# Performance work log

Hardware: AMD Instinct MI355X
Metric: run time of the kernel (lower is better)

Reference implementation:

```python
import jax, jax.numpy as jnp
import numpy as np

N_NODES = 20000
E_RAND = 300000
IN_F, OUT_F, HEADS = 1280, 128, 4
HID = OUT_F * HEADS  # 512


def gat_conv(x, src, dst, W, attn_l, attn_r, bias, n_nodes):
    """DGL GATConv: fc (no bias) -> per-edge LeakyReLU(el_src+er_dst) ->
    segment softmax over incoming edges -> weighted scatter-sum -> +bias.
    Returns (N, HEADS, OUT_F)."""
    h = (x @ W).reshape(n_nodes, HEADS, OUT_F)            # (N,H,F)
    el = jnp.einsum('nhf,hf->nh', h, attn_l)              # (N,H)
    er = jnp.einsum('nhf,hf->nh', h, attn_r)              # (N,H)
    e = jax.nn.leaky_relu(el[src] + er[dst], 0.2)         # (E,H)
    emax = jax.ops.segment_max(e, dst, num_segments=n_nodes)
    ee = jnp.exp(e - emax[dst])                           # (E,H)
    denom = jax.ops.segment_sum(ee, dst, num_segments=n_nodes)
    alpha = ee / denom[dst]                               # (E,H)
    msg = h[src] * alpha[:, :, None]                      # (E,H,F)
    out = jax.ops.segment_sum(msg, dst, num_segments=n_nodes)
    return out + bias.reshape(HEADS, OUT_F)


def setup_inputs() -> dict:
    key = jax.random.key(0)
    ks = jax.random.split(key, 12)
    src_r = jax.random.randint(ks[0], (E_RAND,), 0, N_NODES)
    dst_r = jax.random.randint(ks[1], (E_RAND,), 0, N_NODES)
    self_loop = jnp.arange(N_NODES)
    src = jnp.concatenate([src_r, self_loop])  # self loops: contact[i][i]=1
    dst = jnp.concatenate([dst_r, self_loop])
    feature = jax.random.normal(ks[2], (N_NODES, IN_F), dtype=jnp.float32)
    s1 = 1.0 / np.sqrt(IN_F)
    s2 = 1.0 / np.sqrt(HID)
    return {
        'feature': feature,
        'W1': jax.random.normal(ks[3], (IN_F, HID), dtype=jnp.float32) * s1,
        'al1': jax.random.normal(ks[4], (HEADS, OUT_F), dtype=jnp.float32) * s2,
        'ar1': jax.random.normal(ks[5], (HEADS, OUT_F), dtype=jnp.float32) * s2,
        'b1': jnp.zeros((HID,), dtype=jnp.float32),
        'W2': jax.random.normal(ks[6], (HID, HID), dtype=jnp.float32) * s2,
        'al2': jax.random.normal(ks[7], (HEADS, OUT_F), dtype=jnp.float32) * s2,
        'ar2': jax.random.normal(ks[8], (HEADS, OUT_F), dtype=jnp.float32) * s2,
        'b2': jnp.zeros((HID,), dtype=jnp.float32),
        'Wfc': jax.random.normal(ks[9], (HID, 64), dtype=jnp.float32) * s2,
        'bfc': jnp.zeros((64,), dtype=jnp.float32),
        'src': src,
        'dst': dst,
    }


def reference(feature, W1, al1, ar1, b1, W2, al2, ar2, b2, Wfc, bfc, src, dst):
    n = feature.shape[0]
    out = gat_conv(feature, src, dst, W1, al1, ar1, b1, n)   # (N,4,128)
    out = jax.nn.elu(out).reshape(n, HID)                    # (N,512)
    out = gat_conv(out, src, dst, W2, al2, ar2, b2, n)       # (N,4,128)
    out = jax.nn.elu(out).reshape(n, HID)                    # (N,512)
    out = out @ Wfc + bfc                                    # (N,64)
    out = jax.nn.elu(out[None, :, :])                        # (1,N,64)
    return out
```

## Files before the change

kernel.cpp:

```cpp
#include <hip/hip_runtime.h>
#include <hip/hip_bf16.h>
#include <math.h>

#define HID 512
#define HEADS 4
#define OUTF 128

typedef __attribute__((ext_vector_type(8))) _Float16 f16x8_t;
typedef __attribute__((ext_vector_type(4))) _Float16 f16x4_t;
typedef __attribute__((ext_vector_type(4))) float f32x4_t;

__device__ __forceinline__ void gl_lds16(const void* g, void* l) {
    __builtin_amdgcn_global_load_lds(
        (const __attribute__((address_space(1))) void*)g,
        (__attribute__((address_space(3))) void*)l, 16, 0, 0);
}

__device__ __forceinline__ void stage_plane32(const _Float16* g, int strideE,
    int rbase, int rmax, char* plane, int tid)
{
#pragma unroll
    for (int j = 0; j < 2; ++j) {
        int gci = j * 256 + tid;
        int r = gci >> 2, c = gci & 3;
        int rg = rbase + r; if (rg > rmax) rg = rmax;
        const char* s = (const char*)(g + (size_t)rg * strideE) + ((c ^ ((r >> 1) & 3)) << 4);
        char* d = plane + (j * 256 + (tid & ~63)) * 16;
        gl_lds16(s, d);
    }
}

__device__ __forceinline__ void a32_load(const float* g, int strideE,
    int rbase, int rmax, int tid, int kbase, float4* v)
{
#pragma unroll
    for (int j = 0; j < 2; ++j) {
        int gci = j * 256 + tid;
        int r = gci >> 2, c = gci & 3;
        int rg = rbase + r; if (rg > rmax) rg = rmax;
        const float* s = g + (size_t)rg * strideE + kbase + ((c ^ ((r >> 1) & 3)) << 3);
        v[j * 2]     = *(const float4*)s;
        v[j * 2 + 1] = *(const float4*)(s + 4);
    }
}
__device__ __forceinline__ void a32_write(char* plane, int tid, const float4* v)
{
#pragma unroll
    for (int j = 0; j < 2; ++j) {
        const float4 a = v[j * 2], b = v[j * 2 + 1];
        f16x8_t o;
        o[0] = (_Float16)a.x; o[1] = (_Float16)a.y;
        o[2] = (_Float16)a.z; o[3] = (_Float16)a.w;
        o[4] = (_Float16)b.x; o[5] = (_Float16)b.y;
        o[6] = (_Float16)b.z; o[7] = (_Float16)b.w;
        *(f16x8_t*)(plane + (j * 256 + tid) * 16) = o;
    }
}

__global__ __launch_bounds__(256) void prep_w(const float* __restrict__ W,
    _Float16* __restrict__ Wt, int K, int NC)
{
    __shared__ float tile[32][33];
    const int k0 = blockIdx.x * 32, n0 = blockIdx.y * 32;
    const int t = threadIdx.x;
    {
        int r = t >> 3, c4 = (t & 7) * 4;
        float4 v = *(const float4*)&W[(size_t)(k0 + r) * NC + n0 + c4];
        tile[r][c4] = v.x; tile[r][c4 + 1] = v.y;
        tile[r][c4 + 2] = v.z; tile[r][c4 + 3] = v.w;
    }
    __syncthreads();
    int n = t >> 3, kc = (t & 7) * 4;
#pragma unroll
    for (int i = 0; i < 4; ++i)
        Wt[(size_t)(n0 + n) * K + k0 + kc + i] = (_Float16)tile[kc + i][n];
}

template<int EPI, int OUT16, int ELER, int A32>
__global__ __launch_bounds__(256, 3) void gemm_f16(
    const void* __restrict__ Ap, const _Float16* __restrict__ Bt,
    const float* __restrict__ bias,
    const float* __restrict__ attl, const float* __restrict__ attr,
    float* __restrict__ elp, float* __restrict__ erp,
    void* __restrict__ Cout, int M, int K, int NCOL, int ldC,
    int ncolT, int nwg)
{
    __shared__ char lds[32768];
    const _Float16* Af  = (const _Float16*)Ap;
    const float*    Af32 = (const float*)Ap;
    const int tid = threadIdx.x;
    const int wave = tid >> 6, lane = tid & 63;
    const int wm = wave >> 1, wn = wave & 1;
    const int b = blockIdx.x;
    const int q = nwg >> 3, rr = nwg & 7;
    const int xcd = b & 7, ib = b >> 3;
    const int logical = (xcd < rr ? xcd * (q + 1) : rr * (q + 1) + (xcd - rr) * q) + ib;
    const int bm = (logical / ncolT) * 128, bcol = logical % ncolT;
    const int bn = bcol * 128;
    const int l15 = lane & 15, l4 = lane >> 4;
    const int swz = (l15 >> 1) & 3;

    f32x4_t acc[4][4];
#pragma unroll
    for (int i = 0; i < 4; ++i)
#pragma unroll
        for (int j = 0; j < 4; ++j) acc[i][j] = (f32x4_t){0.f, 0.f, 0.f, 0.f};

    const int nt = K >> 5;
    float4 pre[4];
    if (A32) {
        a32_load(Af32, K, bm, M - 1, tid, 0, pre);
        a32_write(lds, tid, pre);
    } else {
        stage_plane32(Af, K, bm, M - 1, lds, tid);
    }
    stage_plane32(Bt, K, bn, NCOL - 1, lds + 8192, tid);
    __syncthreads();

    for (int t = 0; t < nt; ++t) {
        char* AH = lds + (t & 1) * 16384;
        char* BH = AH + 8192;
        char* AHn = lds + ((t + 1) & 1) * 16384;
        if (t + 1 < nt) {
            if (A32) a32_load(Af32, K, bm, M - 1, tid, (t + 1) * 32, pre);
            else     stage_plane32(Af + (t + 1) * 32, K, bm, M - 1, AHn, tid);
            stage_plane32(Bt + (t + 1) * 32, K, bn, NCOL - 1, AHn + 8192, tid);
        }
        f16x8_t fa[4], fb[4];
#pragma unroll
        for (int mf = 0; mf < 4; ++mf) {
            int row = wm * 64 + mf * 16 + l15;
            fa[mf] = *(const f16x8_t*)(AH + row * 64 + ((l4 ^ swz) << 4));
        }
#pragma unroll
        for (int nf = 0; nf < 4; ++nf) {
            int rn = wn * 64 + nf * 16 + l15;
            fb[nf] = *(const f16x8_t*)(BH + rn * 64 + ((l4 ^ swz) << 4));
        }
#pragma unroll
        for (int mf = 0; mf < 4; ++mf)
#pragma unroll
            for (int nf = 0; nf < 4; ++nf)
                acc[mf][nf] = __builtin_amdgcn_mfma_f32_16x16x32_f16(fa[mf], fb[nf], acc[mf][nf], 0, 0, 0);
        if (A32 && t + 1 < nt) a32_write(AHn, tid, pre);
        __syncthreads();
    }
#pragma unroll
    for (int mf = 0; mf < 4; ++mf) {
        int rbase = bm + wm * 64 + mf * 16 + l4 * 4;
#pragma unroll
        for (int nf = 0; nf < 4; ++nf) {
            int col = bn + wn * 64 + nf * 16 + l15;
            if (col >= NCOL) continue;
#pragma unroll
            for (int r = 0; r < 4; ++r) {
                int row = rbase + r;
                if (row < M) {
                    float v = acc[mf][nf][r];
                    if (EPI) {
                        v += bias[col];
                        v = v > 0.f ? v : (expf(v) - 1.f);
                    }
                    if (OUT16) ((_Float16*)Cout)[(size_t)row * ldC + col] = (_Float16)v;
                    else       ((float*)Cout)[(size_t)row * ldC + col] = v;
                }
            }
        }
    }
    if (ELER) {
        const int head = bcol;
        float alv[4], arv[4];
#pragma unroll
        for (int nf = 0; nf < 4; ++nf) {
            int cl = wn * 64 + nf * 16 + l15;
            alv[nf] = attl[head * OUTF + cl];
            arv[nf] = attr[head * OUTF + cl];
        }
        float pel[4][4], perr[4][4];
#pragma unroll
        for (int mf = 0; mf < 4; ++mf)
#pragma unroll
            for (int r = 0; r < 4; ++r) {
                float se = 0.f, sr = 0.f;
#pragma unroll
                for (int nf = 0; nf < 4; ++nf) {
                    se = fmaf(acc[mf][nf][r], alv[nf], se);
                    sr = fmaf(acc[mf][nf][r], arv[nf], sr);
                }
                pel[mf][r] = se; perr[mf][r] = sr;
            }
#pragma unroll
        for (int off = 1; off < 16; off <<= 1)
#pragma unroll
            for (int mf = 0; mf < 4; ++mf)
#pragma unroll
                for (int r = 0; r < 4; ++r) {
                    pel[mf][r]  += __shfl_xor(pel[mf][r],  off);
                    perr[mf][r] += __shfl_xor(perr[mf][r], off);
                }
        __syncthreads();
        float* red = (float*)lds;
        if (l15 == 0) {
#pragma unroll
            for (int mf = 0; mf < 4; ++mf)
#pragma unroll
                for (int r = 0; r < 4; ++r) {
                    int rl = wm * 64 + mf * 16 + l4 * 4 + r;
                    red[rl * 2 + wn]       = pel[mf][r];
                    red[256 + rl * 2 + wn] = perr[mf][r];
                }
        }
        __syncthreads();
        if (tid < 128) {
            int row = bm + tid;
            if (row < M) {
                float es = red[tid * 2] + red[tid * 2 + 1];
                float rs = red[256 + tid * 2] + red[256 + tid * 2 + 1];
                elp[row * HEADS + head] = es;
                erp[row * HEADS + head] = rs;
            }
        }
    }
}

__global__ void hist_kernel(const int* __restrict__ dst, int* __restrict__ deg, int E)
{
    int e = blockIdx.x * 256 + threadIdx.x;
    if (e < E) atomicAdd(&deg[dst[e]], 1);
}

__global__ __launch_bounds__(256) void scan1_kernel(const int* __restrict__ deg,
    int* __restrict__ offs, int* __restrict__ bsum, int N)
{
    __shared__ int buf[256];
    int tid = threadIdx.x;
    int i = blockIdx.x * 256 + tid;
    int v = (i < N) ? deg[i] : 0;
    buf[tid] = v;
    __syncthreads();
#pragma unroll
    for (int off = 1; off < 256; off <<= 1) {
        int t = (tid >= off) ? buf[tid - off] : 0;
        __syncthreads();
        buf[tid] += t;
        __syncthreads();
    }
    if (i < N) offs[i] = buf[tid] - v;
    if (tid == 255) bsum[blockIdx.x] = buf[255];
}

__global__ void scan2_kernel(int* __restrict__ bsum, int nb)
{
    if (threadIdx.x == 0) {
        int acc = 0;
        for (int b = 0; b < nb; ++b) { int t = bsum[b]; bsum[b] = acc; acc += t; }
        bsum[nb] = acc;
    }
}

__global__ void scan3_kernel(int* __restrict__ offs, const int* __restrict__ bsum,
                             int N, int nb)
{
    int i = blockIdx.x * 256 + threadIdx.x;
    if (i < N) offs[i] += bsum[blockIdx.x];
    if (i == 0) offs[N] = bsum[nb];
}

__global__ void fill_kernel(const int* __restrict__ srcv, const int* __restrict__ dstv,
    const int* __restrict__ offs, int* __restrict__ cursor,
    int* __restrict__ psrc, int E)
{
    int e = blockIdx.x * 256 + threadIdx.x;
    if (e < E) {
        int d = dstv[e];
        int p = atomicAdd(&cursor[d], 1);
        psrc[offs[d] + p] = srcv[e];
    }
}

__global__ __launch_bounds__(256) void aggregate_kernel(const _Float16* __restrict__ h,
    const int* __restrict__ offs, const int* __restrict__ psrc,
    const float* __restrict__ el, const float* __restrict__ er,
    const float* __restrict__ bias, _Float16* __restrict__ xo, int N)
{
    const int n = blockIdx.x * 4 + (threadIdx.x >> 6);
    if (n >= N) return;
    const int lane = threadIdx.x & 63;
    const int c = lane * 8;
    const int head = lane >> 4;
    const int hp = lane >> 5;
    const int e31 = lane & 31;
    const int sbase = (head >> 1) << 5;
    const int hsel = head & 1;

    const float2 er2 = *(const float2*)&er[n * HEADS + hp * 2];

    float acc[8];
#pragma unroll
    for (int k = 0; k < 8; ++k) acc[k] = 0.f;
    float ws = 0.f;

    const int beg = offs[n], end = offs[n + 1];
    for (int base = beg; base < end; base += 32) {
        const int cnt = min(32, end - base);
        int idx = base + e31;
        if (e31 >= cnt) idx = beg;
        const int s = psrc[idx];
        const float2 lv = *(const float2*)&el[s * HEADS + hp * 2];
        float x0 = lv.x + er2.x; x0 = x0 > 0.f ? x0 : 0.2f * x0;
        float x1 = lv.y + er2.y; x1 = x1 > 0.f ? x1 : 0.2f * x1;
        const float wa = expf(x0);
        const float wb = expf(x1);

        int j = 0;
        for (; j + 4 <= cnt; j += 4) {
            int s0 = __shfl(s, j);     int s1 = __shfl(s, j + 1);
            int s2 = __shfl(s, j + 2); int s3 = __shfl(s, j + 3);
            float a0 = __shfl(wa, sbase + j),     b0 = __shfl(wb, sbase + j);
            float a1 = __shfl(wa, sbase + j + 1), b1 = __shfl(wb, sbase + j + 1);
            float a2 = __shfl(wa, sbase + j + 2), b2 = __shfl(wb, sbase + j + 2);
            float a3 = __shfl(wa, sbase + j + 3), b3 = __shfl(wb, sbase + j + 3);
            float w0 = hsel ? b0 : a0;
            float w1 = hsel ? b1 : a1;
            float w2 = hsel ? b2 : a2;
            float w3 = hsel ? b3 : a3;
            f16x8_t v0 = *(const f16x8_t*)&h[(size_t)s0 * HID + c];
            f16x8_t v1 = *(const f16x8_t*)&h[(size_t)s1 * HID + c];
            f16x8_t v2 = *(const f16x8_t*)&h[(size_t)s2 * HID + c];
            f16x8_t v3 = *(const f16x8_t*)&h[(size_t)s3 * HID + c];
#pragma unroll
            for (int k = 0; k < 8; ++k) {
                acc[k] = fmaf(w0, (float)v0[k], acc[k]);
                acc[k] = fmaf(w1, (float)v1[k], acc[k]);
                acc[k] = fmaf(w2, (float)v2[k], acc[k]);
                acc[k] = fmaf(w3, (float)v3[k], acc[k]);
            }
            ws += w0 + w1 + w2 + w3;
        }
        for (; j < cnt; ++j) {
            int s0 = __shfl(s, j);
            float a0 = __shfl(wa, sbase + j), b0 = __shfl(wb, sbase + j);
            float w0 = hsel ? b0 : a0;
            f16x8_t v0 = *(const f16x8_t*)&h[(size_t)s0 * HID + c];
#pragma unroll
            for (int k = 0; k < 8; ++k) acc[k] = fmaf(w0, (float)v0[k], acc[k]);
            ws += w0;
        }
    }
    float inv = 1.f / ws;
    float4 b0v = *(const float4*)&bias[c];
    float4 b1v = *(const float4*)&bias[c + 4];
    float bb[8] = {b0v.x, b0v.y, b0v.z, b0v.w, b1v.x, b1v.y, b1v.z, b1v.w};
    f16x8_t ov;
#pragma unroll
    for (int k = 0; k < 8; ++k) {
        float r = acc[k] * inv + bb[k];
        r = r > 0.f ? r : (expf(r) - 1.f);
        ov[k] = (_Float16)r;
    }
    *(f16x8_t*)&xo[(size_t)n * HID + c] = ov;
}

extern "C" void kernel_launch(void* const* d_in, const int* in_sizes, int n_in,
                              void* d_out, int out_size, void* d_ws, size_t ws_size,
                              hipStream_t stream)
{
    const float* feature = (const float*)d_in[0];
    const float* W1  = (const float*)d_in[1];
    const float* al1 = (const float*)d_in[2];
    const float* ar1 = (const float*)d_in[3];
    const float* b1  = (const float*)d_in[4];
    const float* W2  = (const float*)d_in[5];
    const float* al2 = (const float*)d_in[6];
    const float* ar2 = (const float*)d_in[7];
    const float* b2  = (const float*)d_in[8];
    const float* Wfc = (const float*)d_in[9];
    const float* bfc = (const float*)d_in[10];
    const int* src = (const int*)d_in[11];
    const int* dst = (const int*)d_in[12];
    const int N = in_sizes[0] / 1280;
    const int E = in_sizes[11];
    const int nb = (N + 255) / 256;
    float* out = (float*)d_out;

    char* ws = (char*)d_ws;
    size_t off = 0;
    auto alloc = [&](size_t bytes) {
        void* p = ws + off;
        off += (bytes + 255) & ~(size_t)255;
        return p;
    };
    int* deg    = (int*)alloc((size_t)N * 4);
    int* cursor = (int*)alloc((size_t)N * 4);
    int* offs   = (int*)alloc((size_t)(N + 1) * 4);
    int* bsum   = (int*)alloc((size_t)(nb + 1) * 4);
    float* el   = (float*)alloc((size_t)N * HEADS * 4);
    float* er   = (float*)alloc((size_t)N * HEADS * 4);
    int* psrc   = (int*)alloc((size_t)E * 4);
    _Float16* hbuf  = (_Float16*)alloc((size_t)N * HID * 2);
    _Float16* xh    = (_Float16*)alloc((size_t)N * HID * 2);
    _Float16* W1t   = (_Float16*)alloc((size_t)HID * 1280 * 2);
    _Float16* W2t   = (_Float16*)alloc((size_t)HID * HID * 2);
    _Float16* Wft   = (_Float16*)alloc((size_t)64 * HID * 2);

    hipMemsetAsync(deg, 0, (size_t)N * 4, stream);
    hipMemsetAsync(cursor, 0, (size_t)N * 4, stream);
    hist_kernel<<<(E + 255) / 256, 256, 0, stream>>>(dst, deg, E);
    scan1_kernel<<<nb, 256, 0, stream>>>(deg, offs, bsum, N);
    scan2_kernel<<<1, 64, 0, stream>>>(bsum, nb);
    scan3_kernel<<<nb, 256, 0, stream>>>(offs, bsum, N, nb);
    fill_kernel<<<(E + 255) / 256, 256, 0, stream>>>(src, dst, offs, cursor, psrc, E);

    prep_w<<<dim3(1280 / 32, HID / 32), 256, 0, stream>>>(W1, W1t, 1280, HID);
    prep_w<<<dim3(HID / 32, HID / 32), 256, 0, stream>>>(W2, W2t, HID, HID);
    prep_w<<<dim3(HID / 32, 64 / 32), 256, 0, stream>>>(Wfc, Wft, HID, 64);

    const int nrowT = (N + 127) / 128;
    const int nwgG = nrowT * (HID / 128);
    const int nwgF = nrowT;
    const int aggB = (N + 3) / 4;

    gemm_f16<0, 1, 1, 1><<<nwgG, 256, 0, stream>>>(feature, W1t, nullptr,
                                                   al1, ar1, el, er,
                                                   hbuf, N, 1280, HID, HID,
                                                   HID / 128, nwgG);
    aggregate_kernel<<<aggB, 256, 0, stream>>>(hbuf, offs, psrc, el, er, b1, xh, N);

    gemm_f16<0, 1, 1, 0><<<nwgG, 256, 0, stream>>>(xh, W2t, nullptr,
                                                   al2, ar2, el, er,
                                                   hbuf, N, HID, HID, HID,
                                                   HID / 128, nwgG);
    aggregate_kernel<<<aggB, 256, 0, stream>>>(hbuf, offs, psrc, el, er, b2, xh, N);

    gemm_f16<1, 0, 0, 0><<<nwgF, 256, 0, stream>>>(xh, Wft, bfc,
                                                   nullptr, nullptr, nullptr, nullptr,
                                                   out, N, HID, 64, 64,
                                                   1, nwgF);
}
```

Baseline: 248.2 us.

## Widen GAT GEMM tiles to 128x256 with 512-thread blocks

The GEMM kernel is templated on the N-tile width. The two hidden-layer GEMMs now use 128x256 tiles with 8 waves per block, so each A tile (including the fp32 feature load and convert in layer 1) is read and staged once per two heads instead of once per head. The el/er attention reduction is generalised to write two heads per block. The cost is more LDS per block, fewer blocks in the grid, and a different occupancy target.

```diff
diff --git a/kernel.cpp b/kernel.cpp
--- a/kernel.cpp
+++ b/kernel.cpp
@@ -16,26 +16,29 @@
         (__attribute__((address_space(3))) void*)l, 16, 0, 0);
 }
 
-__device__ __forceinline__ void stage_plane32(const _Float16* g, int strideE,
+template<int ROWS, int THREADS>
+__device__ __forceinline__ void stage_f16(const _Float16* g, int strideE,
     int rbase, int rmax, char* plane, int tid)
 {
-#pragma unroll
-    for (int j = 0; j < 2; ++j) {
-        int gci = j * 256 + tid;
+    constexpr int CH = ROWS * 4;
+#pragma unroll
+    for (int j = 0; j < CH / THREADS; ++j) {
+        int gci = j * THREADS + tid;
         int r = gci >> 2, c = gci & 3;
         int rg = rbase + r; if (rg > rmax) rg = rmax;
         const char* s = (const char*)(g + (size_t)rg * strideE) + ((c ^ ((r >> 1) & 3)) << 4);
-        char* d = plane + (j * 256 + (tid & ~63)) * 16;
+        char* d = plane + (j * THREADS + (tid & ~63)) * 16;
         gl_lds16(s, d);
     }
 }
 
+template<int THREADS>
 __device__ __forceinline__ void a32_load(const float* g, int strideE,
     int rbase, int rmax, int tid, int kbase, float4* v)
 {
 #pragma unroll
-    for (int j = 0; j < 2; ++j) {
-        int gci = j * 256 + tid;
+    for (int j = 0; j < 512 / THREADS; ++j) {
+        int gci = j * THREADS + tid;
         int r = gci >> 2, c = gci & 3;
         int rg = rbase + r; if (rg > rmax) rg = rmax;
         const float* s = g + (size_t)rg * strideE + kbase + ((c ^ ((r >> 1) & 3)) << 3);
@@ -43,17 +46,18 @@
         v[j * 2 + 1] = *(const float4*)(s + 4);
     }
 }
+template<int THREADS>
 __device__ __forceinline__ void a32_write(char* plane, int tid, const float4* v)
 {
 #pragma unroll
-    for (int j = 0; j < 2; ++j) {
+    for (int j = 0; j < 512 / THREADS; ++j) {
         const float4 a = v[j * 2], b = v[j * 2 + 1];
         f16x8_t o;
         o[0] = (_Float16)a.x; o[1] = (_Float16)a.y;
         o[2] = (_Float16)a.z; o[3] = (_Float16)a.w;
         o[4] = (_Float16)b.x; o[5] = (_Float16)b.y;
         o[6] = (_Float16)b.z; o[7] = (_Float16)b.w;
-        *(f16x8_t*)(plane + (j * 256 + tid) * 16) = o;
+        *(f16x8_t*)(plane + (j * THREADS + tid) * 16) = o;
     }
 }
 
@@ -76,8 +80,8 @@
         Wt[(size_t)(n0 + n) * K + k0 + kc + i] = (_Float16)tile[kc + i][n];
 }
 
-template<int EPI, int OUT16, int ELER, int A32>
-__global__ __launch_bounds__(256, 3) void gemm_f16(
+template<int EPI, int OUT16, int ELER, int A32, int BN>
+__global__ __launch_bounds__(BN * 2, BN == 256 ? 4 : 3) void gemm_f16(
     const void* __restrict__ Ap, const _Float16* __restrict__ Bt,
     const float* __restrict__ bias,
     const float* __restrict__ attl, const float* __restrict__ attr,
@@ -85,18 +89,23 @@
     void* __restrict__ Cout, int M, int K, int NCOL, int ldC,
     int ncolT, int nwg)
 {
-    __shared__ char lds[32768];
-    const _Float16* Af  = (const _Float16*)Ap;
+    constexpr int THREADS = BN * 2;
+    constexpr int NWN = BN / 64;
+    constexpr int ABUF = 8192;
+    constexpr int BBUF = BN * 64;
+    constexpr int HBUF = ABUF + BBUF;
+    __shared__ char lds[2 * HBUF];
+    const _Float16* Af   = (const _Float16*)Ap;
     const float*    Af32 = (const float*)Ap;
     const int tid = threadIdx.x;
     const int wave = tid >> 6, lane = tid & 63;
-    const int wm = wave >> 1, wn = wave & 1;
+    const int wm = wave / NWN, wn = wave % NWN;
     const int b = blockIdx.x;
     const int q = nwg >> 3, rr = nwg & 7;
     const int xcd = b & 7, ib = b >> 3;
     const int logical = (xcd < rr ? xcd * (q + 1) : rr * (q + 1) + (xcd - rr) * q) + ib;
     const int bm = (logical / ncolT) * 128, bcol = logical % ncolT;
-    const int bn = bcol * 128;
+    const int bn = bcol * BN;
     const int l15 = lane & 15, l4 = lane >> 4;
     const int swz = (l15 >> 1) & 3;
 
@@ -109,22 +118,22 @@
     const int nt = K >> 5;
     float4 pre[4];
     if (A32) {
-        a32_load(Af32, K, bm, M - 1, tid, 0, pre);
-        a32_write(lds, tid, pre);
+        a32_load<THREADS>(Af32, K, bm, M - 1, tid, 0, pre);
+        a32_write<THREADS>(lds, tid, pre);
     } else {
-        stage_plane32(Af, K, bm, M - 1, lds, tid);
-    }
-    stage_plane32(Bt, K, bn, NCOL - 1, lds + 8192, tid);
+        stage_f16<128, THREADS>(Af, K, bm, M - 1, lds, tid);
+    }
+    stage_f16<BN, THREADS>(Bt, K, bn, NCOL - 1, lds + ABUF, tid);
     __syncthreads();
 
     for (int t = 0; t < nt; ++t) {
-        char* AH = lds + (t & 1) * 16384;
-        char* BH = AH + 8192;
-        char* AHn = lds + ((t + 1) & 1) * 16384;
+        char* AH = lds + (t & 1) * HBUF;
+        char* BH = AH + ABUF;
+        char* AHn = lds + ((t + 1) & 1) * HBUF;
         if (t + 1 < nt) {
-            if (A32) a32_load(Af32, K, bm, M - 1, tid, (t + 1) * 32, pre);
-            else     stage_plane32(Af + (t + 1) * 32, K, bm, M - 1, AHn, tid);
-            stage_plane32(Bt + (t + 1) * 32, K, bn, NCOL - 1, AHn + 8192, tid);
+            if (A32) a32_load<THREADS>(Af32, K, bm, M - 1, tid, (t + 1) * 32, pre);
+            else     stage_f16<128, THREADS>(Af + (t + 1) * 32, K, bm, M - 1, AHn, tid);
+            stage_f16<BN, THREADS>(Bt + (t + 1) * 32, K, bn, NCOL - 1, AHn + ABUF, tid);
         }
         f16x8_t fa[4], fb[4];
 #pragma unroll
@@ -142,7 +151,7 @@
 #pragma unroll
             for (int nf = 0; nf < 4; ++nf)
                 acc[mf][nf] = __builtin_amdgcn_mfma_f32_16x16x32_f16(fa[mf], fb[nf], acc[mf][nf], 0, 0, 0);
-        if (A32 && t + 1 < nt) a32_write(AHn, tid, pre);
+        if (A32 && t + 1 < nt) a32_write<THREADS>(AHn, tid, pre);
         __syncthreads();
     }
 #pragma unroll
@@ -168,11 +177,12 @@
         }
     }
     if (ELER) {
-        const int head = bcol;
+        constexpr int HPT = BN / 128;
+        const int head = bcol * HPT + (wn >> 1);
         float alv[4], arv[4];
 #pragma unroll
         for (int nf = 0; nf < 4; ++nf) {
-            int cl = wn * 64 + nf * 16 + l15;
+            int cl = (wn & 1) * 64 + nf * 16 + l15;
             alv[nf] = attl[head * OUTF + cl];
             arv[nf] = attr[head * OUTF + cl];
         }
@@ -206,18 +216,21 @@
 #pragma unroll
                 for (int r = 0; r < 4; ++r) {
                     int rl = wm * 64 + mf * 16 + l4 * 4 + r;
-                    red[rl * 2 + wn]       = pel[mf][r];
-                    red[256 + rl * 2 + wn] = perr[mf][r];
+                    red[rl * NWN + wn]             = pel[mf][r];
+                    red[128 * NWN + rl * NWN + wn] = perr[mf][r];
                 }
         }
         __syncthreads();
-        if (tid < 128) {
-            int row = bm + tid;
+        if (tid < 128 * HPT) {
+            int rl = tid & 127;
+            int hh = tid >> 7;
+            int row = bm + rl;
             if (row < M) {
-                float es = red[tid * 2] + red[tid * 2 + 1];
-                float rs = red[256 + tid * 2] + red[256 + tid * 2 + 1];
-                elp[row * HEADS + head] = es;
-                erp[row * HEADS + head] = rs;
+                float es = red[rl * NWN + hh * 2] + red[rl * NWN + hh * 2 + 1];
+                float rs = red[128 * NWN + rl * NWN + hh * 2]
+                         + red[128 * NWN + rl * NWN + hh * 2 + 1];
+                elp[row * HEADS + bcol * HPT + hh] = es;
+                erp[row * HEADS + bcol * HPT + hh] = rs;
             }
         }
     }
@@ -416,24 +429,24 @@
     prep_w<<<dim3(HID / 32, 64 / 32), 256, 0, stream>>>(Wfc, Wft, HID, 64);
 
     const int nrowT = (N + 127) / 128;
-    const int nwgG = nrowT * (HID / 128);
+    const int nwgG = nrowT * 2;
     const int nwgF = nrowT;
     const int aggB = (N + 3) / 4;
 
-    gemm_f16<0, 1, 1, 1><<<nwgG, 256, 0, stream>>>(feature, W1t, nullptr,
-                                                   al1, ar1, el, er,
-                                                   hbuf, N, 1280, HID, HID,
-                                                   HID / 128, nwgG);
+    gemm_f16<0, 1, 1, 1, 256><<<nwgG, 512, 0, stream>>>(feature, W1t, nullptr,
+                                                        al1, ar1, el, er,
+                                                        hbuf, N, 1280, HID, HID,
+                                                        2, nwgG);
     aggregate_kernel<<<aggB, 256, 0, stream>>>(hbuf, offs, psrc, el, er, b1, xh, N);
 
-    gemm_f16<0, 1, 1, 0><<<nwgG, 256, 0, stream>>>(xh, W2t, nullptr,
-                                                   al2, ar2, el, er,
-                                                   hbuf, N, HID, HID, HID,
-                                                   HID / 128, nwgG);
+    gemm_f16<0, 1, 1, 0, 256><<<nwgG, 512, 0, stream>>>(xh, W2t, nullptr,
+                                                        al2, ar2, el, er,
+                                                        hbuf, N, HID, HID, HID,
+                                                        2, nwgG);
     aggregate_kernel<<<aggB, 256, 0, stream>>>(hbuf, offs, psrc, el, er, b2, xh, N);
 
-    gemm_f16<1, 0, 0, 0><<<nwgF, 256, 0, stream>>>(xh, Wft, bfc,
-                                                   nullptr, nullptr, nullptr, nullptr,
-                                                   out, N, HID, 64, 64,
-                                                   1, nwgF);
-}
+    gemm_f16<1, 0, 0, 0, 128><<<nwgF, 256, 0, stream>>>(xh, Wft, bfc,
+                                                        nullptr, nullptr, nullptr, nullptr,
+                                                        out, N, HID, 64, 64,
+                                                        1, nwgF);
+}
```

After: 252.7 us. About the same (+1.8%).

## Triple-buffer B tiles with explicit waitcnt barriers in GEMM mainloop

Applied to the files above, without the earlier changes.

The GEMM mainloop now keeps the B operand in a three-slot LDS ring and prefetches two K-steps ahead, while A stays double-buffered. The __syncthreads is replaced by an explicit s_waitcnt vmcnt(2) plus s_barrier, so the newest B load can still be in flight across the barrier. The aim is to hide more global-load latency. LDS grows to 40 KB and launch bounds rise to 4 waves per SIMD, which may force register spills or limit occupancy by LDS; the vmcnt counting assumes each stage_plane32 issues exactly two loads per thread.

```diff
diff --git a/kernel.cpp b/kernel.cpp
--- a/kernel.cpp
+++ b/kernel.cpp
@@ -77,7 +77,7 @@
 }
 
 template<int EPI, int OUT16, int ELER, int A32>
-__global__ __launch_bounds__(256, 3) void gemm_f16(
+__global__ __launch_bounds__(256, 4) void gemm_f16(
     const void* __restrict__ Ap, const _Float16* __restrict__ Bt,
     const float* __restrict__ bias,
     const float* __restrict__ attl, const float* __restrict__ attr,
@@ -85,8 +85,10 @@
     void* __restrict__ Cout, int M, int K, int NCOL, int ldC,
     int ncolT, int nwg)
 {
-    __shared__ char lds[32768];
-    const _Float16* Af  = (const _Float16*)Ap;
+    __shared__ char lds[40960];
+    char* const abase = lds;
+    char* const bbase = lds + 16384;
+    const _Float16* Af   = (const _Float16*)Ap;
     const float*    Af32 = (const float*)Ap;
     const int tid = threadIdx.x;
     const int wave = tid >> 6, lane = tid & 63;
@@ -110,22 +112,33 @@
     float4 pre[4];
     if (A32) {
         a32_load(Af32, K, bm, M - 1, tid, 0, pre);
-        a32_write(lds, tid, pre);
+        a32_write(abase, tid, pre);
     } else {
-        stage_plane32(Af, K, bm, M - 1, lds, tid);
-    }
-    stage_plane32(Bt, K, bn, NCOL - 1, lds + 8192, tid);
-    __syncthreads();
+        stage_plane32(Af, K, bm, M - 1, abase, tid);
+    }
+    stage_plane32(Bt, K, bn, NCOL - 1, bbase, tid);
+    if (nt > 1) {
+        stage_plane32(Bt + 32, K, bn, NCOL - 1, bbase + 8192, tid);
+        asm volatile("s_waitcnt vmcnt(2) lgkmcnt(0)" ::: "memory");
+    } else {
+        asm volatile("s_waitcnt vmcnt(0) lgkmcnt(0)" ::: "memory");
+    }
+    __builtin_amdgcn_sched_barrier(0);
+    __builtin_amdgcn_s_barrier();
+    __builtin_amdgcn_sched_barrier(0);
 
     for (int t = 0; t < nt; ++t) {
-        char* AH = lds + (t & 1) * 16384;
-        char* BH = AH + 8192;
-        char* AHn = lds + ((t + 1) & 1) * 16384;
-        if (t + 1 < nt) {
-            if (A32) a32_load(Af32, K, bm, M - 1, tid, (t + 1) * 32, pre);
-            else     stage_plane32(Af + (t + 1) * 32, K, bm, M - 1, AHn, tid);
-            stage_plane32(Bt + (t + 1) * 32, K, bn, NCOL - 1, AHn + 8192, tid);
-        }
+        char* AH = abase + (t & 1) * 8192;
+        char* BH = bbase + (t % 3) * 8192;
+        if (A32) {
+            if (t + 1 < nt) a32_load(Af32, K, bm, M - 1, tid, (t + 1) * 32, pre);
+        } else if (t + 1 < nt) {
+            stage_plane32(Af + (t + 1) * 32, K, bm, M - 1,
+                          abase + ((t + 1) & 1) * 8192, tid);
+        }
+        if (t + 2 < nt)
+            stage_plane32(Bt + (t + 2) * 32, K, bn, NCOL - 1,
+                          bbase + ((t + 2) % 3) * 8192, tid);
         f16x8_t fa[4], fb[4];
 #pragma unroll
         for (int mf = 0; mf < 4; ++mf) {
@@ -142,8 +155,13 @@
 #pragma unroll
             for (int nf = 0; nf < 4; ++nf)
                 acc[mf][nf] = __builtin_amdgcn_mfma_f32_16x16x32_f16(fa[mf], fb[nf], acc[mf][nf], 0, 0, 0);
-        if (A32 && t + 1 < nt) a32_write(AHn, tid, pre);
-        __syncthreads();
+        if (A32 && t + 1 < nt)
+            a32_write(abase + ((t + 1) & 1) * 8192, tid, pre);
+        if (t + 2 < nt) asm volatile("s_waitcnt vmcnt(2) lgkmcnt(0)" ::: "memory");
+        else            asm volatile("s_waitcnt vmcnt(0) lgkmcnt(0)" ::: "memory");
+        __builtin_amdgcn_sched_barrier(0);
+        __builtin_amdgcn_s_barrier();
+        __builtin_amdgcn_sched_barrier(0);
     }
 #pragma unroll
     for (int mf = 0; mf < 4; ++mf) {
@@ -416,20 +434,20 @@
     prep_w<<<dim3(HID / 32, 64 / 32), 256, 0, stream>>>(Wfc, Wft, HID, 64);
 
     const int nrowT = (N + 127) / 128;
-    const int nwgG = nrowT * (HID / 128);
+    const int nwgG = nrowT * 4;
     const int nwgF = nrowT;
     const int aggB = (N + 3) / 4;
 
     gemm_f16<0, 1, 1, 1><<<nwgG, 256, 0, stream>>>(feature, W1t, nullptr,
                                                    al1, ar1, el, er,
                                                    hbuf, N, 1280, HID, HID,
-                                                   HID / 128, nwgG);
+                                                   4, nwgG);
     aggregate_kernel<<<aggB, 256, 0, stream>>>(hbuf, offs, psrc, el, er, b1, xh, N);
 
     gemm_f16<0, 1, 1, 0><<<nwgG, 256, 0, stream>>>(xh, W2t, nullptr,
                                                    al2, ar2, el, er,
                                                    hbuf, N, HID, HID, HID,
-                                                   HID / 128, nwgG);
+                                                   4, nwgG);
     aggregate_kernel<<<aggB, 256, 0, stream>>>(hbuf, offs, psrc, el, er, b2, xh, N);
 
     gemm_f16<1, 0, 0, 0><<<nwgF, 256, 0, stream>>>(xh, Wft, bfc,
```

Measured after the change: 245.6 us. About the same (-1.0%).
